# Optimization experiments

Measured on AMD Instinct MI355X. Metric: run time of the kernel, lower is better.

## Reference

```python
import jax, jax.numpy as jnp
import numpy as np

N_NODES = 100000
N_EDGES = 1000000
D_IN = 64
D_OUT = 64


def setup_inputs() -> dict:
    key = jax.random.key(0)
    k_feat, k_ei, k_ew, k_w, k_b = jax.random.split(key, 5)
    features = jax.random.normal(k_feat, (N_NODES, D_IN), dtype=jnp.float32)
    edge_index = jax.random.randint(k_ei, (2, N_EDGES), 0, N_NODES, dtype=jnp.int64)
    edge_weight = jax.random.uniform(k_ew, (N_EDGES,), dtype=jnp.float32)
    # nn.Linear(input_dim, output_dim): weight [out, in], bias [out]
    lim = 1.0 / np.sqrt(D_IN)
    W = jax.random.uniform(k_w, (D_OUT, D_IN), minval=-lim, maxval=lim, dtype=jnp.float32)
    b = jax.random.uniform(k_b, (D_OUT,), minval=-lim, maxval=lim, dtype=jnp.float32)
    return {"features": features, "edge_index": edge_index,
            "edge_weight": edge_weight, "W": W, "b": b}


def reference(features, edge_index, edge_weight, W, b):
    # gather source-node features and scale by edge weight: [E, F]
    messages = features[edge_index[0]] * edge_weight[:, None]
    # scatter-add into destination nodes (vectorized form of the per-column
    # scatter_add_ loop in the original): [N, F]
    aggregated = jax.ops.segment_sum(messages, edge_index[1],
                                     num_segments=features.shape[0])
    # residual + linear; dropout is identity in eval mode
    return (aggregated + features) @ W.T + b
```

## Files before the change

kernel.cpp:

```cpp
#include <hip/hip_runtime.h>

constexpr int N_NODES = 100000;
constexpr int N_EDGES = 1000000;
constexpr int D = 64;
constexpr int NTILES = (N_NODES + 1023) / 1024;
constexpr int CAP1 = 16;
constexpr int CAP2 = 16;
constexpr int OVF_CAP = 65536;
constexpr int NXCD = 8;
constexpr int NODES_PER_GRP = 12500;


__global__ __launch_bounds__(256) void build_k(
    const int*   __restrict__ ei,
    const float* __restrict__ ew,
    int*         __restrict__ cnt,
    unsigned*    __restrict__ b16,
    unsigned*    __restrict__ b32,
    int*         __restrict__ ovfCount,
    int4*        __restrict__ ovf)
{
    int grp  = blockIdx.x & 7;
    int gidx = blockIdx.x >> 3;
    int lo   = grp * NODES_PER_GRP;
    int hi   = lo + NODES_PER_GRP;
    int stride = (gridDim.x >> 3) * 256;

    for (int e = gidx * 256 + threadIdx.x; e < N_EDGES; e += stride) {
        int dst = ei[N_EDGES + e];
        if (dst < lo || dst >= hi) continue;
        int   src = ei[e];
        float w   = ew[e];
        unsigned rec = ((unsigned)src << 15) | (unsigned)(w * 32767.0f + 0.5f);
        int pos = atomicAdd(&cnt[dst], 1);
        if (pos < CAP1) {
            b16[dst * 16 + pos] = rec;
        } else if (pos < CAP1 + CAP2) {
            b32[dst * 16 + (pos - CAP1)] = rec;
        } else {
            int oi = atomicAdd(ovfCount, 1);
            if (oi < OVF_CAP) ovf[oi] = make_int4(dst, src, __float_as_int(w), 0);
        }
    }
}

__global__ __launch_bounds__(256) void agg_gemm_bucket_k(
    const float*    __restrict__ feat,
    const unsigned* __restrict__ b16,
    const unsigned* __restrict__ b32,
    const int*      __restrict__ cnt,
    const int*      __restrict__ ovfCount,
    const int4*     __restrict__ ovf,
    const float*    __restrict__ W,
    const float*    __restrict__ bias,
    float*          __restrict__ out)
{
    constexpr int PITCH = 68;
    constexpr int NPB = 16;
    __shared__ float Wl[D * PITCH];
    __shared__ float xs[NPB][D];

    int tid = threadIdx.x;
    for (int i = tid; i < D * D; i += 256)
        Wl[(i >> 6) * PITCH + (i & 63)] = W[i];

    int lane = tid & 63;
    int wv   = tid >> 6;
    int g    = lane >> 4;
    int sub  = lane & 15;

    int slot = wv * 4 + g;
    int n    = blockIdx.x * NPB + slot;

    float4 acc = *reinterpret_cast<const float4*>(feat + (size_t)n * D + sub * 4);

    int degRaw = cnt[n];
    int deg = degRaw > CAP1 ? CAP1 : degRaw;
    const unsigned* ep = b16 + (size_t)n * 16;
#pragma unroll 2
    for (int j = 0; j < deg; ++j) {
        unsigned r = ep[j];
        float w  = (float)(r & 0x7FFFu) * (1.0f / 32767.0f);
        int   s  = (int)(r >> 15);
        float4 f = *reinterpret_cast<const float4*>(
            feat + (size_t)s * D + sub * 4);
        acc.x = fmaf(f.x, w, acc.x);
        acc.y = fmaf(f.y, w, acc.y);
        acc.z = fmaf(f.z, w, acc.z);
        acc.w = fmaf(f.w, w, acc.w);
    }
    if (degRaw > CAP1) {
        int d2 = (degRaw > CAP1 + CAP2 ? CAP1 + CAP2 : degRaw) - CAP1;
        const unsigned* ep2 = b32 + (size_t)n * 16;
        for (int j = 0; j < d2; ++j) {
            unsigned r = ep2[j];
            float w  = (float)(r & 0x7FFFu) * (1.0f / 32767.0f);
            int   s  = (int)(r >> 15);
            float4 f = *reinterpret_cast<const float4*>(
                feat + (size_t)s * D + sub * 4);
            acc.x = fmaf(f.x, w, acc.x);
            acc.y = fmaf(f.y, w, acc.y);
            acc.z = fmaf(f.z, w, acc.z);
            acc.w = fmaf(f.w, w, acc.w);
        }
        if (degRaw > CAP1 + CAP2) {
            int m = *ovfCount;
            if (m > OVF_CAP) m = OVF_CAP;
            for (int i = 0; i < m; ++i) {
                int4 r = ovf[i];
                if (r.x == n) {
                    float w  = __int_as_float(r.z);
                    float4 f = *reinterpret_cast<const float4*>(
                        feat + (size_t)r.y * D + sub * 4);
                    acc.x = fmaf(f.x, w, acc.x);
                    acc.y = fmaf(f.y, w, acc.y);
                    acc.z = fmaf(f.z, w, acc.z);
                    acc.w = fmaf(f.w, w, acc.w);
                }
            }
        }
    }
    *reinterpret_cast<float4*>(&xs[slot][sub * 4]) = acc;
    __syncthreads();

    const float4* w4 = reinterpret_cast<const float4*>(&Wl[lane * PITCH]);
    const float4* x0 = reinterpret_cast<const float4*>(&xs[wv * 4 + 0][0]);
    const float4* x1 = reinterpret_cast<const float4*>(&xs[wv * 4 + 1][0]);
    const float4* x2 = reinterpret_cast<const float4*>(&xs[wv * 4 + 2][0]);
    const float4* x3 = reinterpret_cast<const float4*>(&xs[wv * 4 + 3][0]);
    float b = bias[lane];
    float a0 = b, a1 = b, a2 = b, a3 = b;
#pragma unroll
    for (int i = 0; i < 16; ++i) {
        float4 wq = w4[i];
        float4 v0 = x0[i];
        float4 v1 = x1[i];
        float4 v2 = x2[i];
        float4 v3 = x3[i];
        a0 += v0.x * wq.x + v0.y * wq.y + v0.z * wq.z + v0.w * wq.w;
        a1 += v1.x * wq.x + v1.y * wq.y + v1.z * wq.z + v1.w * wq.w;
        a2 += v2.x * wq.x + v2.y * wq.y + v2.z * wq.z + v2.w * wq.w;
        a3 += v3.x * wq.x + v3.y * wq.y + v3.z * wq.z + v3.w * wq.w;
    }
    int nb = blockIdx.x * NPB + wv * 4;
    out[(size_t)(nb + 0) * D + lane] = a0;
    out[(size_t)(nb + 1) * D + lane] = a1;
    out[(size_t)(nb + 2) * D + lane] = a2;
    out[(size_t)(nb + 3) * D + lane] = a3;
}


__global__ __launch_bounds__(256) void rank_k(
    const int* __restrict__ ei, int* __restrict__ cnt, int* __restrict__ rank)
{
    int e = blockIdx.x * 256 + threadIdx.x;
    if (e >= N_EDGES) return;
    rank[e] = atomicAdd(&cnt[ei[N_EDGES + e]], 1);
}

__global__ __launch_bounds__(256) void tile_sum_k(
    const int* __restrict__ counts, int* __restrict__ tileSums)
{
    __shared__ int red[256];
    int t = threadIdx.x;
    int base = blockIdx.x * 1024 + t * 4;
    int4 c = make_int4(0, 0, 0, 0);
    if (base + 3 < N_NODES) {
        c = *reinterpret_cast<const int4*>(counts + base);
    } else {
        if (base + 0 < N_NODES) c.x = counts[base + 0];
        if (base + 1 < N_NODES) c.y = counts[base + 1];
        if (base + 2 < N_NODES) c.z = counts[base + 2];
        if (base + 3 < N_NODES) c.w = counts[base + 3];
    }
    red[t] = c.x + c.y + c.z + c.w;
    __syncthreads();
    for (int d = 128; d > 0; d >>= 1) {
        if (t < d) red[t] += red[t + d];
        __syncthreads();
    }
    if (t == 0) tileSums[blockIdx.x] = red[0];
}

__global__ __launch_bounds__(128) void tile_scan_k(
    const int* __restrict__ tileSums, int* __restrict__ tileBase)
{
    __shared__ int s[128];
    int t = threadIdx.x;
    s[t] = (t < NTILES) ? tileSums[t] : 0;
    __syncthreads();
    for (int d = 1; d < 128; d <<= 1) {
        int v = (t >= d) ? s[t - d] : 0;
        __syncthreads();
        s[t] += v;
        __syncthreads();
    }
    if (t < NTILES) tileBase[t] = t ? s[t - 1] : 0;
}

__global__ __launch_bounds__(256) void scan_apply_k(
    int* __restrict__ counts, const int* __restrict__ tileBase,
    int* __restrict__ offsets)
{
    __shared__ int tsum[256];
    int t = threadIdx.x;
    int base = blockIdx.x * 1024 + t * 4;
    int4 c = make_int4(0, 0, 0, 0);
    bool full = (base + 3 < N_NODES);
    if (full) {
        c = *reinterpret_cast<const int4*>(counts + base);
    } else {
        if (base + 0 < N_NODES) c.x = counts[base + 0];
        if (base + 1 < N_NODES) c.y = counts[base + 1];
        if (base + 2 < N_NODES) c.z = counts[base + 2];
        if (base + 3 < N_NODES) c.w = counts[base + 3];
    }
    tsum[t] = c.x + c.y + c.z + c.w;
    __syncthreads();
    for (int d = 1; d < 256; d <<= 1) {
        int v = (t >= d) ? tsum[t - d] : 0;
        __syncthreads();
        tsum[t] += v;
        __syncthreads();
    }
    int run = tileBase[blockIdx.x] + (t ? tsum[t - 1] : 0);
    int4 o = make_int4(run, run + c.x, run + c.x + c.y, run + c.x + c.y + c.z);
    if (full) {
        *reinterpret_cast<int4*>(offsets + base) = o;
        *reinterpret_cast<int4*>(counts  + base) = o;
    } else {
        if (base + 0 < N_NODES) { offsets[base + 0] = o.x; counts[base + 0] = o.x; }
        if (base + 1 < N_NODES) { offsets[base + 1] = o.y; counts[base + 1] = o.y; }
        if (base + 2 < N_NODES) { offsets[base + 2] = o.z; counts[base + 2] = o.z; }
        if (base + 3 < N_NODES) { offsets[base + 3] = o.w; counts[base + 3] = o.w; }
    }
    if (blockIdx.x == 0 && t == 0) offsets[N_NODES] = N_EDGES;
}

__global__ __launch_bounds__(256) void place_k(
    const int*   __restrict__ ei,
    const float* __restrict__ ew,
    const int*   __restrict__ rank,
    const int*   __restrict__ offsets,
    int2*        __restrict__ sorted_e)
{
    int e = blockIdx.x * 256 + threadIdx.x;
    if (e >= N_EDGES) return;
    int dst = ei[N_EDGES + e];
    int pos = offsets[dst] + rank[e];
    sorted_e[pos] = make_int2(ei[e], __float_as_int(ew[e]));
}

__global__ __launch_bounds__(256) void agg_gemm_k(
    const float* __restrict__ feat,
    const int2*  __restrict__ sorted_e,
    const int*   __restrict__ offsets,
    const float* __restrict__ W,
    const float* __restrict__ bias,
    float*       __restrict__ out)
{
    constexpr int PITCH = 68;
    constexpr int NPB = 16;
    __shared__ float Wl[D * PITCH];
    __shared__ float xs[NPB][D];

    int tid = threadIdx.x;
    for (int i = tid; i < D * D; i += 256)
        Wl[(i >> 6) * PITCH + (i & 63)] = W[i];

    int lane = tid & 63;
    int wv   = tid >> 6;
    int g    = lane >> 4;
    int sub  = lane & 15;

    int slot = wv * 4 + g;
    int n    = blockIdx.x * NPB + slot;
    int lo = offsets[n], hi = offsets[n + 1];
    int deg = hi - lo;

    float4 acc = *reinterpret_cast<const float4*>(feat + (size_t)n * D + sub * 4);

    const int2* ep = sorted_e + lo;
#pragma unroll 2
    for (int j = 0; j < deg; ++j) {
        int2  er = ep[j];
        float w  = __int_as_float(er.y);
        float4 f = *reinterpret_cast<const float4*>(
            feat + (size_t)er.x * D + sub * 4);
        acc.x = fmaf(f.x, w, acc.x);
        acc.y = fmaf(f.y, w, acc.y);
        acc.z = fmaf(f.z, w, acc.z);
        acc.w = fmaf(f.w, w, acc.w);
    }
    *reinterpret_cast<float4*>(&xs[slot][sub * 4]) = acc;
    __syncthreads();

    const float4* w4 = reinterpret_cast<const float4*>(&Wl[lane * PITCH]);
    const float4* x0 = reinterpret_cast<const float4*>(&xs[wv * 4 + 0][0]);
    const float4* x1 = reinterpret_cast<const float4*>(&xs[wv * 4 + 1][0]);
    const float4* x2 = reinterpret_cast<const float4*>(&xs[wv * 4 + 2][0]);
    const float4* x3 = reinterpret_cast<const float4*>(&xs[wv * 4 + 3][0]);
    float b = bias[lane];
    float a0 = b, a1 = b, a2 = b, a3 = b;
#pragma unroll
    for (int i = 0; i < 16; ++i) {
        float4 wq = w4[i];
        float4 v0 = x0[i];
        float4 v1 = x1[i];
        float4 v2 = x2[i];
        float4 v3 = x3[i];
        a0 += v0.x * wq.x + v0.y * wq.y + v0.z * wq.z + v0.w * wq.w;
        a1 += v1.x * wq.x + v1.y * wq.y + v1.z * wq.z + v1.w * wq.w;
        a2 += v2.x * wq.x + v2.y * wq.y + v2.z * wq.z + v2.w * wq.w;
        a3 += v3.x * wq.x + v3.y * wq.y + v3.z * wq.z + v3.w * wq.w;
    }
    int nb = blockIdx.x * NPB + wv * 4;
    out[(size_t)(nb + 0) * D + lane] = a0;
    out[(size_t)(nb + 1) * D + lane] = a1;
    out[(size_t)(nb + 2) * D + lane] = a2;
    out[(size_t)(nb + 3) * D + lane] = a3;
}


__global__ __launch_bounds__(256) void scatter_k(
    const float* __restrict__ feat,
    const int*   __restrict__ ei,
    const float* __restrict__ ew,
    float*       __restrict__ agg)
{
    int gid = blockIdx.x * 256 + threadIdx.x;
    int e = gid >> 4;
    if (e >= N_EDGES) return;
    int c = (gid & 15) * 4;
    int   src = ei[e];
    int   dst = ei[N_EDGES + e];
    float w   = ew[e];
    float4 f = *reinterpret_cast<const float4*>(feat + (size_t)src * D + c);
    float* a = agg + (size_t)dst * D + c;
    atomicAdd(a + 0, f.x * w);
    atomicAdd(a + 1, f.y * w);
    atomicAdd(a + 2, f.z * w);
    atomicAdd(a + 3, f.w * w);
}

__global__ __launch_bounds__(256) void gemm_k(
    const float* __restrict__ agg,
    const float* __restrict__ feat,
    const float* __restrict__ W,
    const float* __restrict__ bias,
    float*       __restrict__ out)
{
    constexpr int PITCH = 68;
    __shared__ float Wl[D * PITCH];
    __shared__ float xs[4][D];
    int tid = threadIdx.x;
    for (int i = tid; i < D * D; i += 256)
        Wl[(i >> 6) * PITCH + (i & 63)] = W[i];
    int o  = tid & 63;
    int wv = tid >> 6;
    int n  = blockIdx.x * 4 + wv;
    float b = bias[o];
    if (n < N_NODES)
        xs[wv][o] = agg[(size_t)n * D + o] + feat[(size_t)n * D + o];
    __syncthreads();
    if (n >= N_NODES) return;
    const float4* x4 = reinterpret_cast<const float4*>(&xs[wv][0]);
    const float4* w4 = reinterpret_cast<const float4*>(&Wl[o * PITCH]);
    float acc = b;
#pragma unroll
    for (int i = 0; i < 16; ++i) {
        float4 xv = x4[i];
        float4 wq = w4[i];
        acc += xv.x * wq.x + xv.y * wq.y + xv.z * wq.z + xv.w * wq.w;
    }
    out[(size_t)n * D + o] = acc;
}


extern "C" void kernel_launch(void* const* d_in, const int* in_sizes, int n_in,
                              void* d_out, int out_size, void* d_ws, size_t ws_size,
                              hipStream_t stream) {
    const float* feat = (const float*)d_in[0];
    const int*   ei   = (const int*)d_in[1];
    const float* ew   = (const float*)d_in[2];
    const float* W    = (const float*)d_in[3];
    const float* b    = (const float*)d_in[4];
    float*       out  = (float*)d_out;

    constexpr size_t NPAD = 100352;

    constexpr size_t CNT_OFF   = 0;
    constexpr size_t B16_OFF   = NPAD * sizeof(int);
    constexpr size_t B32_OFF   = B16_OFF + (size_t)N_NODES * 16 * sizeof(unsigned);
    constexpr size_t OVF_OFF   = B32_OFF + (size_t)N_NODES * 16 * sizeof(unsigned);
    constexpr size_t WS_BUCKET = OVF_OFF + (size_t)OVF_CAP * sizeof(int4);

    constexpr size_t OFFSET_OFF = NPAD * sizeof(int);
    constexpr size_t RANK_OFF   = 2 * NPAD * sizeof(int);
    constexpr size_t SORT_OFF   = RANK_OFF + (size_t)N_EDGES * sizeof(int);
    constexpr size_t WS_SORT    = SORT_OFF + (size_t)N_EDGES * sizeof(int2);

    if (ws_size >= WS_BUCKET) {
        int*      cnt      = (int*)((char*)d_ws + CNT_OFF);
        int*      ovfCount = cnt + 100104;
        unsigned* b16      = (unsigned*)((char*)d_ws + B16_OFF);
        unsigned* b32      = (unsigned*)((char*)d_ws + B32_OFF);
        int4*     ovf      = (int4*)((char*)d_ws + OVF_OFF);

        hipMemsetAsync(cnt, 0, (100104 + 1) * sizeof(int), stream);
        build_k<<<512, 256, 0, stream>>>(ei, ew, cnt, b16, b32, ovfCount, ovf);
        agg_gemm_bucket_k<<<N_NODES / 16, 256, 0, stream>>>(
            feat, b16, b32, cnt, ovfCount, ovf, W, b, out);
    } else if (ws_size >= WS_SORT) {
        int*  cnt      = (int*)((char*)d_ws + CNT_OFF);
        int*  offsets  = (int*)((char*)d_ws + OFFSET_OFF);
        int*  rank     = (int*)((char*)d_ws + RANK_OFF);
        int2* sorted_e = (int2*)((char*)d_ws + SORT_OFF);
        int*  tileSums = cnt + 100096;
        int*  tileBase = cnt + 100224;

        hipMemsetAsync(cnt, 0, N_NODES * sizeof(int), stream);
        rank_k     <<<(N_EDGES + 255) / 256, 256, 0, stream>>>(ei, cnt, rank);
        tile_sum_k <<<NTILES, 256, 0, stream>>>(cnt, tileSums);
        tile_scan_k<<<1, 128, 0, stream>>>(tileSums, tileBase);
        scan_apply_k<<<NTILES, 256, 0, stream>>>(cnt, tileBase, offsets);
        place_k    <<<(N_EDGES + 255) / 256, 256, 0, stream>>>(ei, ew, rank, offsets, sorted_e);
        agg_gemm_k <<<N_NODES / 16, 256, 0, stream>>>(feat, sorted_e, offsets, W, b, out);
    } else {
        const size_t agg_bytes = (size_t)N_NODES * D * sizeof(float);
        float* agg = (ws_size >= agg_bytes) ? (float*)d_ws : out;
        hipMemsetAsync(agg, 0, agg_bytes, stream);
        scatter_k<<<(N_EDGES * 16) / 256, 256, 0, stream>>>(feat, ei, ew, agg);
        gemm_k<<<(N_NODES + 3) / 4, 256, 0, stream>>>(agg, feat, W, b, out);
    }
}
```

Measured before the change: 197.3 us.

## Fuse bucket build and aggregate-GEMM into one cooperative persistent kernel

Replaces the memset + build_k + agg_gemm_bucket_k launch sequence with a single cooperative kernel. It zeroes the counters, builds per-node edge buckets, and then runs a persistent tile loop for aggregation and the 64x64 GEMM, with grid.sync between phases. The build phase reads destinations as int4 and packs source and weight into 15-bit quantized records. W is staged into LDS only once per block. This removes launch gaps and the per-block W reload, but adds grid-wide barriers, a fixed grid of 1792 blocks that relies on 7 blocks per CU fitting, and it drops the sort-based fallback path.

```diff
diff --git a/kernel.cpp b/kernel.cpp
--- a/kernel.cpp
+++ b/kernel.cpp
@@ -1,14 +1,168 @@
 #include <hip/hip_runtime.h>
+#include <hip/hip_cooperative_groups.h>
+
+namespace cg = cooperative_groups;
 
 constexpr int N_NODES = 100000;
 constexpr int N_EDGES = 1000000;
 constexpr int D = 64;
-constexpr int NTILES = (N_NODES + 1023) / 1024;
 constexpr int CAP1 = 16;
 constexpr int CAP2 = 16;
 constexpr int OVF_CAP = 65536;
-constexpr int NXCD = 8;
 constexpr int NODES_PER_GRP = 12500;
+constexpr int GRID_FUSED = 1792;
+
+__global__ __launch_bounds__(256, 7) void fused_k(
+    const float* __restrict__ feat,
+    const int*   __restrict__ ei,
+    const float* __restrict__ ew,
+    const float* __restrict__ W,
+    const float* __restrict__ bias,
+    int*         __restrict__ cnt,
+    unsigned*    __restrict__ b16,
+    unsigned*    __restrict__ b32,
+    int*         __restrict__ ovfCount,
+    int4*        __restrict__ ovf,
+    float*       __restrict__ out)
+{
+    cg::grid_group grid = cg::this_grid();
+    constexpr int PITCH = 68;
+    constexpr int NPB = 16;
+    __shared__ float Wl[D * PITCH];
+    __shared__ float xs[NPB][D];
+
+    int tid  = threadIdx.x;
+    int gtid = blockIdx.x * 256 + tid;
+    int gsz  = gridDim.x * 256;
+
+    for (int i = gtid; i < 100112; i += gsz) cnt[i] = 0;
+    for (int i = tid; i < D * D; i += 256)
+        Wl[(i >> 6) * PITCH + (i & 63)] = W[i];
+    grid.sync();
+
+    {
+        int grp  = blockIdx.x & 7;
+        int lo   = grp * NODES_PER_GRP;
+        int hi   = lo + NODES_PER_GRP;
+        int bpg  = gridDim.x >> 3;
+        int gidx = blockIdx.x >> 3;
+        const int4* dst4 = reinterpret_cast<const int4*>(ei + N_EDGES);
+        int nquad = N_EDGES / 4;
+        for (int q = gidx * 256 + tid; q < nquad; q += bpg * 256) {
+            int4 d4 = dst4[q];
+            int e0 = q * 4;
+#pragma unroll
+            for (int k = 0; k < 4; ++k) {
+                int dst = (&d4.x)[k];
+                if (dst < lo || dst >= hi) continue;
+                int e = e0 + k;
+                int   src = ei[e];
+                float w   = ew[e];
+                unsigned rec = ((unsigned)src << 15) |
+                               (unsigned)(w * 32767.0f + 0.5f);
+                int pos = atomicAdd(&cnt[dst], 1);
+                if (pos < CAP1) {
+                    b16[dst * 16 + pos] = rec;
+                } else if (pos < CAP1 + CAP2) {
+                    b32[dst * 16 + (pos - CAP1)] = rec;
+                } else {
+                    int oi = atomicAdd(ovfCount, 1);
+                    if (oi < OVF_CAP)
+                        ovf[oi] = make_int4(dst, src, __float_as_int(w), 0);
+                }
+            }
+        }
+    }
+    grid.sync();
+
+    int lane = tid & 63;
+    int wv   = tid >> 6;
+    int g    = lane >> 4;
+    int sub  = lane & 15;
+    int slot = wv * 4 + g;
+
+    for (int tile = blockIdx.x; tile < N_NODES / NPB; tile += gridDim.x) {
+        int n = tile * NPB + slot;
+
+        float4 acc = *reinterpret_cast<const float4*>(
+            feat + (size_t)n * D + sub * 4);
+
+        int degRaw = cnt[n];
+        int deg = degRaw > CAP1 ? CAP1 : degRaw;
+        const unsigned* ep = b16 + (size_t)n * 16;
+#pragma unroll 2
+        for (int j = 0; j < deg; ++j) {
+            unsigned r = ep[j];
+            float w  = (float)(r & 0x7FFFu) * (1.0f / 32767.0f);
+            int   s  = (int)(r >> 15);
+            float4 f = *reinterpret_cast<const float4*>(
+                feat + (size_t)s * D + sub * 4);
+            acc.x = fmaf(f.x, w, acc.x);
+            acc.y = fmaf(f.y, w, acc.y);
+            acc.z = fmaf(f.z, w, acc.z);
+            acc.w = fmaf(f.w, w, acc.w);
+        }
+        if (degRaw > CAP1) {
+            int d2 = (degRaw > CAP1 + CAP2 ? CAP1 + CAP2 : degRaw) - CAP1;
+            const unsigned* ep2 = b32 + (size_t)n * 16;
+            for (int j = 0; j < d2; ++j) {
+                unsigned r = ep2[j];
+                float w  = (float)(r & 0x7FFFu) * (1.0f / 32767.0f);
+                int   s  = (int)(r >> 15);
+                float4 f = *reinterpret_cast<const float4*>(
+                    feat + (size_t)s * D + sub * 4);
+                acc.x = fmaf(f.x, w, acc.x);
+                acc.y = fmaf(f.y, w, acc.y);
+                acc.z = fmaf(f.z, w, acc.z);
+                acc.w = fmaf(f.w, w, acc.w);
+            }
+            if (degRaw > CAP1 + CAP2) {
+                int m = *ovfCount;
+                if (m > OVF_CAP) m = OVF_CAP;
+                for (int i = 0; i < m; ++i) {
+                    int4 r = ovf[i];
+                    if (r.x == n) {
+                        float w  = __int_as_float(r.z);
+                        float4 f = *reinterpret_cast<const float4*>(
+                            feat + (size_t)r.y * D + sub * 4);
+                        acc.x = fmaf(f.x, w, acc.x);
+                        acc.y = fmaf(f.y, w, acc.y);
+                        acc.z = fmaf(f.z, w, acc.z);
+                        acc.w = fmaf(f.w, w, acc.w);
+                    }
+                }
+            }
+        }
+        *reinterpret_cast<float4*>(&xs[slot][sub * 4]) = acc;
+        __syncthreads();
+
+        const float4* w4 = reinterpret_cast<const float4*>(&Wl[lane * PITCH]);
+        const float4* x0 = reinterpret_cast<const float4*>(&xs[wv * 4 + 0][0]);
+        const float4* x1 = reinterpret_cast<const float4*>(&xs[wv * 4 + 1][0]);
+        const float4* x2 = reinterpret_cast<const float4*>(&xs[wv * 4 + 2][0]);
+        const float4* x3 = reinterpret_cast<const float4*>(&xs[wv * 4 + 3][0]);
+        float b = bias[lane];
+        float a0 = b, a1 = b, a2 = b, a3 = b;
+#pragma unroll
+        for (int i = 0; i < 16; ++i) {
+            float4 wq = w4[i];
+            float4 v0 = x0[i];
+            float4 v1 = x1[i];
+            float4 v2 = x2[i];
+            float4 v3 = x3[i];
+            a0 += v0.x * wq.x + v0.y * wq.y + v0.z * wq.z + v0.w * wq.w;
+            a1 += v1.x * wq.x + v1.y * wq.y + v1.z * wq.z + v1.w * wq.w;
+            a2 += v2.x * wq.x + v2.y * wq.y + v2.z * wq.z + v2.w * wq.w;
+            a3 += v3.x * wq.x + v3.y * wq.y + v3.z * wq.z + v3.w * wq.w;
+        }
+        int nb = tile * NPB + wv * 4;
+        out[(size_t)(nb + 0) * D + lane] = a0;
+        out[(size_t)(nb + 1) * D + lane] = a1;
+        out[(size_t)(nb + 2) * D + lane] = a2;
+        out[(size_t)(nb + 3) * D + lane] = a3;
+        __syncthreads();
+    }
+}
 
 
 __global__ __launch_bounds__(256) void build_k(
@@ -119,178 +273,6 @@
                 }
             }
         }
-    }
-    *reinterpret_cast<float4*>(&xs[slot][sub * 4]) = acc;
-    __syncthreads();
-
-    const float4* w4 = reinterpret_cast<const float4*>(&Wl[lane * PITCH]);
-    const float4* x0 = reinterpret_cast<const float4*>(&xs[wv * 4 + 0][0]);
-    const float4* x1 = reinterpret_cast<const float4*>(&xs[wv * 4 + 1][0]);
-    const float4* x2 = reinterpret_cast<const float4*>(&xs[wv * 4 + 2][0]);
-    const float4* x3 = reinterpret_cast<const float4*>(&xs[wv * 4 + 3][0]);
-    float b = bias[lane];
-    float a0 = b, a1 = b, a2 = b, a3 = b;
-#pragma unroll
-    for (int i = 0; i < 16; ++i) {
-        float4 wq = w4[i];
-        float4 v0 = x0[i];
-        float4 v1 = x1[i];
-        float4 v2 = x2[i];
-        float4 v3 = x3[i];
-        a0 += v0.x * wq.x + v0.y * wq.y + v0.z * wq.z + v0.w * wq.w;
-        a1 += v1.x * wq.x + v1.y * wq.y + v1.z * wq.z + v1.w * wq.w;
-        a2 += v2.x * wq.x + v2.y * wq.y + v2.z * wq.z + v2.w * wq.w;
-        a3 += v3.x * wq.x + v3.y * wq.y + v3.z * wq.z + v3.w * wq.w;
-    }
-    int nb = blockIdx.x * NPB + wv * 4;
-    out[(size_t)(nb + 0) * D + lane] = a0;
-    out[(size_t)(nb + 1) * D + lane] = a1;
-    out[(size_t)(nb + 2) * D + lane] = a2;
-    out[(size_t)(nb + 3) * D + lane] = a3;
-}
-
-
-__global__ __launch_bounds__(256) void rank_k(
-    const int* __restrict__ ei, int* __restrict__ cnt, int* __restrict__ rank)
-{
-    int e = blockIdx.x * 256 + threadIdx.x;
-    if (e >= N_EDGES) return;
-    rank[e] = atomicAdd(&cnt[ei[N_EDGES + e]], 1);
-}
-
-__global__ __launch_bounds__(256) void tile_sum_k(
-    const int* __restrict__ counts, int* __restrict__ tileSums)
-{
-    __shared__ int red[256];
-    int t = threadIdx.x;
-    int base = blockIdx.x * 1024 + t * 4;
-    int4 c = make_int4(0, 0, 0, 0);
-    if (base + 3 < N_NODES) {
-        c = *reinterpret_cast<const int4*>(counts + base);
-    } else {
-        if (base + 0 < N_NODES) c.x = counts[base + 0];
-        if (base + 1 < N_NODES) c.y = counts[base + 1];
-        if (base + 2 < N_NODES) c.z = counts[base + 2];
-        if (base + 3 < N_NODES) c.w = counts[base + 3];
-    }
-    red[t] = c.x + c.y + c.z + c.w;
-    __syncthreads();
-    for (int d = 128; d > 0; d >>= 1) {
-        if (t < d) red[t] += red[t + d];
-        __syncthreads();
-    }
-    if (t == 0) tileSums[blockIdx.x] = red[0];
-}
-
-__global__ __launch_bounds__(128) void tile_scan_k(
-    const int* __restrict__ tileSums, int* __restrict__ tileBase)
-{
-    __shared__ int s[128];
-    int t = threadIdx.x;
-    s[t] = (t < NTILES) ? tileSums[t] : 0;
-    __syncthreads();
-    for (int d = 1; d < 128; d <<= 1) {
-        int v = (t >= d) ? s[t - d] : 0;
-        __syncthreads();
-        s[t] += v;
-        __syncthreads();
-    }
-    if (t < NTILES) tileBase[t] = t ? s[t - 1] : 0;
-}
-
-__global__ __launch_bounds__(256) void scan_apply_k(
-    int* __restrict__ counts, const int* __restrict__ tileBase,
-    int* __restrict__ offsets)
-{
-    __shared__ int tsum[256];
-    int t = threadIdx.x;
-    int base = blockIdx.x * 1024 + t * 4;
-    int4 c = make_int4(0, 0, 0, 0);
-    bool full = (base + 3 < N_NODES);
-    if (full) {
-        c = *reinterpret_cast<const int4*>(counts + base);
-    } else {
-        if (base + 0 < N_NODES) c.x = counts[base + 0];
-        if (base + 1 < N_NODES) c.y = counts[base + 1];
-        if (base + 2 < N_NODES) c.z = counts[base + 2];
-        if (base + 3 < N_NODES) c.w = counts[base + 3];
-    }
-    tsum[t] = c.x + c.y + c.z + c.w;
-    __syncthreads();
-    for (int d = 1; d < 256; d <<= 1) {
-        int v = (t >= d) ? tsum[t - d] : 0;
-        __syncthreads();
-        tsum[t] += v;
-        __syncthreads();
-    }
-    int run = tileBase[blockIdx.x] + (t ? tsum[t - 1] : 0);
-    int4 o = make_int4(run, run + c.x, run + c.x + c.y, run + c.x + c.y + c.z);
-    if (full) {
-        *reinterpret_cast<int4*>(offsets + base) = o;
-        *reinterpret_cast<int4*>(counts  + base) = o;
-    } else {
-        if (base + 0 < N_NODES) { offsets[base + 0] = o.x; counts[base + 0] = o.x; }
-        if (base + 1 < N_NODES) { offsets[base + 1] = o.y; counts[base + 1] = o.y; }
-        if (base + 2 < N_NODES) { offsets[base + 2] = o.z; counts[base + 2] = o.z; }
-        if (base + 3 < N_NODES) { offsets[base + 3] = o.w; counts[base + 3] = o.w; }
-    }
-    if (blockIdx.x == 0 && t == 0) offsets[N_NODES] = N_EDGES;
-}
-
-__global__ __launch_bounds__(256) void place_k(
-    const int*   __restrict__ ei,
-    const float* __restrict__ ew,
-    const int*   __restrict__ rank,
-    const int*   __restrict__ offsets,
-    int2*        __restrict__ sorted_e)
-{
-    int e = blockIdx.x * 256 + threadIdx.x;
-    if (e >= N_EDGES) return;
-    int dst = ei[N_EDGES + e];
-    int pos = offsets[dst] + rank[e];
-    sorted_e[pos] = make_int2(ei[e], __float_as_int(ew[e]));
-}
-
-__global__ __launch_bounds__(256) void agg_gemm_k(
-    const float* __restrict__ feat,
-    const int2*  __restrict__ sorted_e,
-    const int*   __restrict__ offsets,
-    const float* __restrict__ W,
-    const float* __restrict__ bias,
-    float*       __restrict__ out)
-{
-    constexpr int PITCH = 68;
-    constexpr int NPB = 16;
-    __shared__ float Wl[D * PITCH];
-    __shared__ float xs[NPB][D];
-
-    int tid = threadIdx.x;
-    for (int i = tid; i < D * D; i += 256)
-        Wl[(i >> 6) * PITCH + (i & 63)] = W[i];
-
-    int lane = tid & 63;
-    int wv   = tid >> 6;
-    int g    = lane >> 4;
-    int sub  = lane & 15;
-
-    int slot = wv * 4 + g;
-    int n    = blockIdx.x * NPB + slot;
-    int lo = offsets[n], hi = offsets[n + 1];
-    int deg = hi - lo;
-
-    float4 acc = *reinterpret_cast<const float4*>(feat + (size_t)n * D + sub * 4);
-
-    const int2* ep = sorted_e + lo;
-#pragma unroll 2
-    for (int j = 0; j < deg; ++j) {
-        int2  er = ep[j];
-        float w  = __int_as_float(er.y);
-        float4 f = *reinterpret_cast<const float4*>(
-            feat + (size_t)er.x * D + sub * 4);
-        acc.x = fmaf(f.x, w, acc.x);
-        acc.y = fmaf(f.y, w, acc.y);
-        acc.z = fmaf(f.z, w, acc.z);
-        acc.w = fmaf(f.w, w, acc.w);
     }
     *reinterpret_cast<float4*>(&xs[slot][sub * 4]) = acc;
     __syncthreads();
@@ -388,17 +370,11 @@
     float*       out  = (float*)d_out;
 
     constexpr size_t NPAD = 100352;
-
     constexpr size_t CNT_OFF   = 0;
     constexpr size_t B16_OFF   = NPAD * sizeof(int);
     constexpr size_t B32_OFF   = B16_OFF + (size_t)N_NODES * 16 * sizeof(unsigned);
     constexpr size_t OVF_OFF   = B32_OFF + (size_t)N_NODES * 16 * sizeof(unsigned);
     constexpr size_t WS_BUCKET = OVF_OFF + (size_t)OVF_CAP * sizeof(int4);
-
-    constexpr size_t OFFSET_OFF = NPAD * sizeof(int);
-    constexpr size_t RANK_OFF   = 2 * NPAD * sizeof(int);
-    constexpr size_t SORT_OFF   = RANK_OFF + (size_t)N_EDGES * sizeof(int);
-    constexpr size_t WS_SORT    = SORT_OFF + (size_t)N_EDGES * sizeof(int2);
 
     if (ws_size >= WS_BUCKET) {
         int*      cnt      = (int*)((char*)d_ws + CNT_OFF);
@@ -407,25 +383,17 @@
         unsigned* b32      = (unsigned*)((char*)d_ws + B32_OFF);
         int4*     ovf      = (int4*)((char*)d_ws + OVF_OFF);
 
-        hipMemsetAsync(cnt, 0, (100104 + 1) * sizeof(int), stream);
-        build_k<<<512, 256, 0, stream>>>(ei, ew, cnt, b16, b32, ovfCount, ovf);
-        agg_gemm_bucket_k<<<N_NODES / 16, 256, 0, stream>>>(
-            feat, b16, b32, cnt, ovfCount, ovf, W, b, out);
-    } else if (ws_size >= WS_SORT) {
-        int*  cnt      = (int*)((char*)d_ws + CNT_OFF);
-        int*  offsets  = (int*)((char*)d_ws + OFFSET_OFF);
-        int*  rank     = (int*)((char*)d_ws + RANK_OFF);
-        int2* sorted_e = (int2*)((char*)d_ws + SORT_OFF);
-        int*  tileSums = cnt + 100096;
-        int*  tileBase = cnt + 100224;
-
-        hipMemsetAsync(cnt, 0, N_NODES * sizeof(int), stream);
-        rank_k     <<<(N_EDGES + 255) / 256, 256, 0, stream>>>(ei, cnt, rank);
-        tile_sum_k <<<NTILES, 256, 0, stream>>>(cnt, tileSums);
-        tile_scan_k<<<1, 128, 0, stream>>>(tileSums, tileBase);
-        scan_apply_k<<<NTILES, 256, 0, stream>>>(cnt, tileBase, offsets);
-        place_k    <<<(N_EDGES + 255) / 256, 256, 0, stream>>>(ei, ew, rank, offsets, sorted_e);
-        agg_gemm_k <<<N_NODES / 16, 256, 0, stream>>>(feat, sorted_e, offsets, W, b, out);
+        void* args[] = {(void*)&feat, (void*)&ei, (void*)&ew, (void*)&W,
+                        (void*)&b, (void*)&cnt, (void*)&b16, (void*)&b32,
+                        (void*)&ovfCount, (void*)&ovf, (void*)&out};
+        hipError_t err = hipLaunchCooperativeKernel(
+            (const void*)fused_k, dim3(GRID_FUSED), dim3(256), args, 0, stream);
+        if (err != hipSuccess) {
+            hipMemsetAsync(cnt, 0, (100104 + 1) * sizeof(int), stream);
+            build_k<<<512, 256, 0, stream>>>(ei, ew, cnt, b16, b32, ovfCount, ovf);
+            agg_gemm_bucket_k<<<N_NODES / 16, 256, 0, stream>>>(
+                feat, b16, b32, cnt, ovfCount, ovf, W, b, out);
+        }
     } else {
         const size_t agg_bytes = (size_t)N_NODES * D * sizeof(float);
         float* agg = (ws_size >= agg_bytes) ? (float*)d_ws : out;
```

Result: slower. 470.4 us (+138.4%).
